# Kernel optimization log

Hardware: AMD Instinct MI355X
Metric: run time of the kernel (lower is better)

## Reference

```python
import jax, jax.numpy as jnp
import numpy as np
from jax import lax

NUM_HEADS = 8
KERNEL_SIZE = 7
PADDING_L = 3
EPS = 1e-12


def pow2_quantize(w):
    # LinearShift: weights constrained to sign * 2^round(log2|w|) (bit-shift arithmetic),
    # with straight-through estimator for gradients.
    wq = jnp.sign(w) * jnp.exp2(jnp.round(jnp.log2(jnp.abs(w) + EPS)))
    return w + lax.stop_gradient(wq - w)


def setup_inputs() -> dict:
    key = jax.random.key(0)
    k1, k2, k3 = jax.random.split(key, 3)
    T, B, C = 4096, 16, 512
    x = jax.random.normal(k1, (T, B, C), dtype=jnp.float32)
    shift_W = jax.random.normal(k2, (C, C), dtype=jnp.float32) * (1.0 / np.sqrt(C))
    shift_b = jnp.zeros((C,), dtype=jnp.float32)
    # xavier-uniform-ish init for the light-conv weight (H, K)
    lim = np.sqrt(6.0 / (NUM_HEADS + KERNEL_SIZE))
    weight = jax.random.uniform(k3, (NUM_HEADS, KERNEL_SIZE), minval=-lim, maxval=lim, dtype=jnp.float32)
    return {"x": x, "shift_W": shift_W, "shift_b": shift_b, "weight": weight}


def reference(x, shift_W, shift_b, weight):
    T, B, C = x.shape
    H, K = weight.shape
    R = C // H
    # 1) shift-linear: power-of-two quantized weights, y = x @ Wq^T + b  (T,B,C)
    Wq = pow2_quantize(shift_W)
    y = jnp.einsum("tbc,dc->tbd", x, Wq) + shift_b
    # 2) light (depthwise, head-shared) convolution along time
    xc = jnp.transpose(y, (1, 2, 0))  # (B, C, T)
    w = jax.nn.softmax(weight, axis=-1)  # weight_softmax=True
    # expand head kernels to per-channel depthwise kernels: (C, 1, K)
    w_full = jnp.repeat(w, R, axis=0)[:, None, :]
    out = lax.conv_general_dilated(
        xc, w_full,
        window_strides=(1,),
        padding=[(PADDING_L, K - 1 - PADDING_L)],
        dimension_numbers=("NCH", "OIH", "NCH"),
        feature_group_count=C,
    )  # (B, C, T)
    return jnp.transpose(out, (2, 0, 1))  # (T, B, C)
```

## Files before the change

kernel.cpp:

```cpp
#include <hip/hip_runtime.h>

constexpr int T_DIM = 4096;
constexpr int B_DIM = 16;
constexpr int C_DIM = 512;
constexpr int K_CONV = 7;
constexpr int M_DIM = T_DIM * B_DIM;
constexpr int BC = B_DIM * C_DIM;

typedef __attribute__((ext_vector_type(8))) short bf16x8;
typedef __attribute__((ext_vector_type(4))) float f32x4;
typedef __attribute__((ext_vector_type(8))) float f32x8;
typedef __attribute__((ext_vector_type(4))) unsigned int u32x4;

__device__ __forceinline__ unsigned short f2bf(float f) {
  unsigned u = __float_as_uint(f);
  u += 0x7fffu + ((u >> 16) & 1u);
  return (unsigned short)(u >> 16);
}
__device__ __forceinline__ unsigned pack2(float a, float b) {
  return (unsigned)f2bf(a) | (((unsigned)f2bf(b)) << 16);
}

__global__ __launch_bounds__(256) void quantize_w(
    const float* __restrict__ W, unsigned short* __restrict__ Wq) {
  int i = blockIdx.x * 256 + threadIdx.x;
  float w = W[i];
  float a = fabsf(w) + 1e-12f;
  float q = exp2f(rintf(log2f(a)));
  q = (w > 0.f) ? q : ((w < 0.f) ? -q : 0.f);
  Wq[i] = f2bf(q);
}

constexpr int BK = 32;
constexpr int NSTEP = C_DIM / BK;

__global__ __launch_bounds__(256, 4) void gemm_bt(
    const float* __restrict__ X, const short* __restrict__ Bt,
    const float* __restrict__ bias, unsigned short* __restrict__ Y) {
  constexpr int K = C_DIM, N = C_DIM;
  __shared__ __align__(16) short As[2][128 * BK];
  __shared__ __align__(16) short Bs[2][128 * BK];

  const int id   = blockIdx.x;
  const int xcd  = id & 7;
  const int slot = id >> 3;
  const int nb   = slot & 3;
  const int mb   = xcd * 64 + (slot >> 2);
  const int m0 = mb * 128;
  const int n0 = nb * 128;

  const int t    = threadIdx.x;
  const int lane = t & 63;
  const int wid  = t >> 6;

  const int ar = t >> 2;
  const int ac = (t & 3) * 8;
  const float* pA = X + (long)(m0 + ar) * K + ac;
  const int awoff = (((t & 3) ^ ((ar >> 1) & 3)) << 4);

  const int bc = ((t & 3) ^ ((t >> 3) & 3)) * 8;
  const short* pB = Bt + (long)(n0 + (t >> 2)) * K + bc;

  const int fr = lane & 15;
  const int fq = lane >> 4;
  const int wm = (wid >> 1) * 64;
  const int wn = (wid & 1) * 64;
  const int sw = ((fq ^ ((fr >> 1) & 3)) << 4);

  f32x4 ax[4];
  f32x4 acc[4][4] = {};

  auto loadA = [&](int k0) {
    ax[0] = *(const f32x4*)(pA + k0);
    ax[1] = *(const f32x4*)(pA + k0 + 4);
    ax[2] = *(const f32x4*)(pA + (long)64 * K + k0);
    ax[3] = *(const f32x4*)(pA + (long)64 * K + k0 + 4);
  };
  auto stageB = [&](int bsel, int k0) {
#pragma unroll
    for (int i = 0; i < 2; ++i)
      __builtin_amdgcn_global_load_lds(
          (const __attribute__((address_space(1))) void*)(pB + (long)i * 64 * K + k0),
          (__attribute__((address_space(3))) void*)&Bs[bsel][i * 2048 + wid * 512],
          16, 0, 0);
  };
  auto writeA = [&](int bsel) {
    char* base = (char*)&As[bsel][0];
    u32x4 p0, p1;
    p0[0] = pack2(ax[0][0], ax[0][1]);
    p0[1] = pack2(ax[0][2], ax[0][3]);
    p0[2] = pack2(ax[1][0], ax[1][1]);
    p0[3] = pack2(ax[1][2], ax[1][3]);
    p1[0] = pack2(ax[2][0], ax[2][1]);
    p1[1] = pack2(ax[2][2], ax[2][3]);
    p1[2] = pack2(ax[3][0], ax[3][1]);
    p1[3] = pack2(ax[3][2], ax[3][3]);
    *(u32x4*)(base + ar * 64 + awoff)        = p0;
    *(u32x4*)(base + (64 + ar) * 64 + awoff) = p1;
  };
  auto compute = [&](int bsel) {
    const char* ab = (const char*)&As[bsel][0];
    const char* bb = (const char*)&Bs[bsel][0];
    bf16x8 af[4], bfr[4];
#pragma unroll
    for (int i = 0; i < 4; ++i)
      af[i] = *(const bf16x8*)(ab + (wm + i * 16 + fr) * 64 + sw);
#pragma unroll
    for (int j = 0; j < 4; ++j)
      bfr[j] = *(const bf16x8*)(bb + (wn + j * 16 + fr) * 64 + sw);
#pragma unroll
    for (int i = 0; i < 4; ++i)
#pragma unroll
      for (int j = 0; j < 4; ++j)
        acc[i][j] = __builtin_amdgcn_mfma_f32_16x16x32_bf16(af[i], bfr[j], acc[i][j], 0, 0, 0);
  };

  loadA(0);
  stageB(0, 0);
  writeA(0);
  __syncthreads();

#pragma unroll
  for (int s = 0; s < NSTEP; ++s) {
    const int buf = s & 1;
    if (s + 1 < NSTEP) {
      loadA((s + 1) * BK);
      stageB(buf ^ 1, (s + 1) * BK);
    }
    compute(buf);
    if (s + 1 < NSTEP) {
      writeA(buf ^ 1);
      __syncthreads();
    }
  }

#pragma unroll
  for (int j = 0; j < 4; ++j) {
    const int gn = n0 + wn + j * 16 + fr;
    const float bv = bias[gn];
#pragma unroll
    for (int i = 0; i < 4; ++i) {
#pragma unroll
      for (int r = 0; r < 4; ++r) {
        const int gm = m0 + wm + i * 16 + fq * 4 + r;
        Y[(long)gm * N + gn] = f2bf(acc[i][j][r] + bv);
      }
    }
  }
}

__device__ __forceinline__ u32x4 loadY(const unsigned short* Y, int t, long off) {
  if ((unsigned)t < (unsigned)T_DIM)
    return *(const u32x4*)(Y + (long)t * BC + off);
  u32x4 z = {0u, 0u, 0u, 0u};
  return z;
}

__device__ __forceinline__ f32x8 unpack8(u32x4 u) {
  f32x8 r;
#pragma unroll
  for (int i = 0; i < 4; ++i) {
    unsigned w = u[i];
    r[2 * i]     = __uint_as_float(w << 16);
    r[2 * i + 1] = __uint_as_float(w & 0xffff0000u);
  }
  return r;
}

__global__ __launch_bounds__(256, 4) void lconv(
    const unsigned short* __restrict__ Y, const float* __restrict__ W,
    float* __restrict__ O) {
  __shared__ float sm_wf[8 * K_CONV];
  if (threadIdx.x < 8) {
    const int h = threadIdx.x;
    float v[K_CONV];
    float mx = -1e30f;
#pragma unroll
    for (int k = 0; k < K_CONV; ++k) { v[k] = W[h * K_CONV + k]; mx = fmaxf(mx, v[k]); }
    float s = 0.f;
#pragma unroll
    for (int k = 0; k < K_CONV; ++k) { v[k] = __expf(v[k] - mx); s += v[k]; }
    const float inv = 1.f / s;
#pragma unroll
    for (int k = 0; k < K_CONV; ++k) sm_wf[h * K_CONV + k] = v[k] * inv;
  }

  const int id   = blockIdx.x;
  const int xcd  = id & 7;
  const int slot = id >> 3;
  const int b    = slot >> 7;
  const int tl   = slot & 127;
  const int t    = xcd * 512 + tl * 4 + (threadIdx.x >> 6);
  const int cvec = threadIdx.x & 63;
  const long off = (long)b * C_DIM + cvec * 8;
  const int h    = cvec >> 3;

  u32x4 v[K_CONV];
#pragma unroll
  for (int k = 0; k < K_CONV; ++k) v[k] = loadY(Y, t + k - 3, off);

  __syncthreads();
  float wf[K_CONV];
#pragma unroll
  for (int k = 0; k < K_CONV; ++k) wf[k] = sm_wf[h * K_CONV + k];

  f32x8 acc = unpack8(v[0]) * wf[0];
#pragma unroll
  for (int k = 1; k < K_CONV; ++k) acc += unpack8(v[k]) * wf[k];

  float* op = O + (long)t * BC + off;
  *(f32x4*)op       = f32x4{acc[0], acc[1], acc[2], acc[3]};
  *(f32x4*)(op + 4) = f32x4{acc[4], acc[5], acc[6], acc[7]};
}

extern "C" void kernel_launch(void* const* d_in, const int* in_sizes, int n_in,
                              void* d_out, int out_size, void* d_ws, size_t ws_size,
                              hipStream_t stream) {
  const float* x       = (const float*)d_in[0];
  const float* shift_W = (const float*)d_in[1];
  const float* shift_b = (const float*)d_in[2];
  const float* weight  = (const float*)d_in[3];
  float* out = (float*)d_out;

  unsigned short* Wq = (unsigned short*)d_ws;
  unsigned short* Y  = Wq + C_DIM * C_DIM;

  quantize_w<<<(C_DIM * C_DIM) / 256, 256, 0, stream>>>(shift_W, Wq);
  gemm_bt<<<(M_DIM / 128) * (C_DIM / 128), 256, 0, stream>>>(
      x, (const short*)Wq, shift_b, Y);
  lconv<<<M_DIM * (C_DIM / 8) / 256, 256, 0, stream>>>(Y, weight, out);
}
```

Baseline: 296.6 us.

## Use 8-wave GEMM blocks and time-chunked light conv with register reuse

The GEMM block grows from 256 to 512 threads, so each of 8 waves computes a 64x32 sub-tile instead of 64x64 and each thread loads half as much A and B per step. This lowers register pressure and raises occupancy, but it also lowers the MFMA-to-LDS-read ratio per wave. The light conv kernel now has each thread compute 8 consecutive timesteps from 14 loaded rows instead of loading 7 rows per output. That removes most of the redundant overlapping Y reads, at the cost of more registers per thread and fewer blocks.

```diff
diff --git a/kernel.cpp b/kernel.cpp
--- a/kernel.cpp
+++ b/kernel.cpp
@@ -34,7 +34,7 @@
 constexpr int BK = 32;
 constexpr int NSTEP = C_DIM / BK;
 
-__global__ __launch_bounds__(256, 4) void gemm_bt(
+__global__ __launch_bounds__(512, 6) void gemm_bt(
     const float* __restrict__ X, const short* __restrict__ Bt,
     const float* __restrict__ bias, unsigned short* __restrict__ Y) {
   constexpr int K = C_DIM, N = C_DIM;
@@ -54,64 +54,54 @@
   const int wid  = t >> 6;
 
   const int ar = t >> 2;
-  const int ac = (t & 3) * 8;
-  const float* pA = X + (long)(m0 + ar) * K + ac;
+  const float* pA = X + (long)(m0 + ar) * K + (t & 3) * 8;
   const int awoff = (((t & 3) ^ ((ar >> 1) & 3)) << 4);
 
-  const int bc = ((t & 3) ^ ((t >> 3) & 3)) * 8;
-  const short* pB = Bt + (long)(n0 + (t >> 2)) * K + bc;
+  const int bc = ((lane & 3) ^ ((lane >> 3) & 3)) * 8;
+  const short* pB = Bt + (long)(n0 + wid * 16 + (lane >> 2)) * K + bc;
 
   const int fr = lane & 15;
   const int fq = lane >> 4;
-  const int wm = (wid >> 1) * 64;
-  const int wn = (wid & 1) * 64;
+  const int wm = (wid >> 2) * 64;
+  const int wn = (wid & 3) * 32;
   const int sw = ((fq ^ ((fr >> 1) & 3)) << 4);
 
-  f32x4 ax[4];
-  f32x4 acc[4][4] = {};
+  f32x4 ax[2];
+  f32x4 acc[4][2] = {};
 
   auto loadA = [&](int k0) {
     ax[0] = *(const f32x4*)(pA + k0);
     ax[1] = *(const f32x4*)(pA + k0 + 4);
-    ax[2] = *(const f32x4*)(pA + (long)64 * K + k0);
-    ax[3] = *(const f32x4*)(pA + (long)64 * K + k0 + 4);
   };
   auto stageB = [&](int bsel, int k0) {
-#pragma unroll
-    for (int i = 0; i < 2; ++i)
-      __builtin_amdgcn_global_load_lds(
-          (const __attribute__((address_space(1))) void*)(pB + (long)i * 64 * K + k0),
-          (__attribute__((address_space(3))) void*)&Bs[bsel][i * 2048 + wid * 512],
-          16, 0, 0);
+    __builtin_amdgcn_global_load_lds(
+        (const __attribute__((address_space(1))) void*)(pB + k0),
+        (__attribute__((address_space(3))) void*)&Bs[bsel][wid * 512],
+        16, 0, 0);
   };
   auto writeA = [&](int bsel) {
     char* base = (char*)&As[bsel][0];
-    u32x4 p0, p1;
-    p0[0] = pack2(ax[0][0], ax[0][1]);
-    p0[1] = pack2(ax[0][2], ax[0][3]);
-    p0[2] = pack2(ax[1][0], ax[1][1]);
-    p0[3] = pack2(ax[1][2], ax[1][3]);
-    p1[0] = pack2(ax[2][0], ax[2][1]);
-    p1[1] = pack2(ax[2][2], ax[2][3]);
-    p1[2] = pack2(ax[3][0], ax[3][1]);
-    p1[3] = pack2(ax[3][2], ax[3][3]);
-    *(u32x4*)(base + ar * 64 + awoff)        = p0;
-    *(u32x4*)(base + (64 + ar) * 64 + awoff) = p1;
+    u32x4 p;
+    p[0] = pack2(ax[0][0], ax[0][1]);
+    p[1] = pack2(ax[0][2], ax[0][3]);
+    p[2] = pack2(ax[1][0], ax[1][1]);
+    p[3] = pack2(ax[1][2], ax[1][3]);
+    *(u32x4*)(base + ar * 64 + awoff) = p;
   };
   auto compute = [&](int bsel) {
     const char* ab = (const char*)&As[bsel][0];
     const char* bb = (const char*)&Bs[bsel][0];
-    bf16x8 af[4], bfr[4];
+    bf16x8 af[4], bfr[2];
 #pragma unroll
     for (int i = 0; i < 4; ++i)
       af[i] = *(const bf16x8*)(ab + (wm + i * 16 + fr) * 64 + sw);
 #pragma unroll
-    for (int j = 0; j < 4; ++j)
+    for (int j = 0; j < 2; ++j)
       bfr[j] = *(const bf16x8*)(bb + (wn + j * 16 + fr) * 64 + sw);
 #pragma unroll
     for (int i = 0; i < 4; ++i)
 #pragma unroll
-      for (int j = 0; j < 4; ++j)
+      for (int j = 0; j < 2; ++j)
         acc[i][j] = __builtin_amdgcn_mfma_f32_16x16x32_bf16(af[i], bfr[j], acc[i][j], 0, 0, 0);
   };
 
@@ -135,7 +125,7 @@
   }
 
 #pragma unroll
-  for (int j = 0; j < 4; ++j) {
+  for (int j = 0; j < 2; ++j) {
     const int gn = n0 + wn + j * 16 + fr;
     const float bv = bias[gn];
 #pragma unroll
@@ -149,6 +139,8 @@
   }
 }
 
+constexpr int CHT = 8;
+
 __device__ __forceinline__ u32x4 loadY(const unsigned short* Y, int t, long off) {
   if ((unsigned)t < (unsigned)T_DIM)
     return *(const u32x4*)(Y + (long)t * BC + off);
@@ -167,7 +159,7 @@
   return r;
 }
 
-__global__ __launch_bounds__(256, 4) void lconv(
+__global__ __launch_bounds__(256, 6) void lconv(
     const unsigned short* __restrict__ Y, const float* __restrict__ W,
     float* __restrict__ O) {
   __shared__ float sm_wf[8 * K_CONV];
@@ -188,29 +180,31 @@
   const int id   = blockIdx.x;
   const int xcd  = id & 7;
   const int slot = id >> 3;
-  const int b    = slot >> 7;
-  const int tl   = slot & 127;
-  const int t    = xcd * 512 + tl * 4 + (threadIdx.x >> 6);
+  const int b    = slot >> 4;
+  const int tl   = slot & 15;
+  const int t0   = xcd * 512 + tl * 32 + (threadIdx.x >> 6) * CHT;
   const int cvec = threadIdx.x & 63;
   const long off = (long)b * C_DIM + cvec * 8;
   const int h    = cvec >> 3;
 
-  u32x4 v[K_CONV];
-#pragma unroll
-  for (int k = 0; k < K_CONV; ++k) v[k] = loadY(Y, t + k - 3, off);
+  u32x4 v[CHT + 6];
+#pragma unroll
+  for (int k = 0; k < CHT + 6; ++k) v[k] = loadY(Y, t0 - 3 + k, off);
 
   __syncthreads();
   float wf[K_CONV];
 #pragma unroll
   for (int k = 0; k < K_CONV; ++k) wf[k] = sm_wf[h * K_CONV + k];
 
-  f32x8 acc = unpack8(v[0]) * wf[0];
-#pragma unroll
-  for (int k = 1; k < K_CONV; ++k) acc += unpack8(v[k]) * wf[k];
-
-  float* op = O + (long)t * BC + off;
-  *(f32x4*)op       = f32x4{acc[0], acc[1], acc[2], acc[3]};
-  *(f32x4*)(op + 4) = f32x4{acc[4], acc[5], acc[6], acc[7]};
+#pragma unroll
+  for (int j = 0; j < CHT; ++j) {
+    f32x8 acc = unpack8(v[j]) * wf[0];
+#pragma unroll
+    for (int k = 1; k < K_CONV; ++k) acc += unpack8(v[j + k]) * wf[k];
+    float* op = O + (long)(t0 + j) * BC + off;
+    *(f32x4*)op       = f32x4{acc[0], acc[1], acc[2], acc[3]};
+    *(f32x4*)(op + 4) = f32x4{acc[4], acc[5], acc[6], acc[7]};
+  }
 }
 
 extern "C" void kernel_launch(void* const* d_in, const int* in_sizes, int n_in,
@@ -226,7 +220,7 @@
   unsigned short* Y  = Wq + C_DIM * C_DIM;
 
   quantize_w<<<(C_DIM * C_DIM) / 256, 256, 0, stream>>>(shift_W, Wq);
-  gemm_bt<<<(M_DIM / 128) * (C_DIM / 128), 256, 0, stream>>>(
+  gemm_bt<<<(M_DIM / 128) * (C_DIM / 128), 512, 0, stream>>>(
       x, (const short*)Wq, shift_b, Y);
-  lconv<<<M_DIM * (C_DIM / 8) / 256, 256, 0, stream>>>(Y, weight, out);
-}
+  lconv<<<M_DIM / CHT * (C_DIM / 8) / 256, 256, 0, stream>>>(Y, weight, out);
+}
```

After: 339.4 us. 1.14x slower.

## Triple-buffer GEMM shared-memory tiles with two-step-ahead prefetch and manual waitcnts

Applied to the files above, without the earlier changes.

The GEMM moves from double to triple buffering in LDS, issuing global loads for A and B two K-steps ahead. It uses explicit vmcnt/lgkmcnt waits and raw s_barrier instead of __syncthreads so more memory latency can overlap the MFMA work. Bias loads are hoisted to the kernel start. In exchange it needs more LDS and registers (occupancy hint drops from 4 to 3), and it depends on hand-counted vmcnt values being correct.

```diff
diff --git a/kernel.cpp b/kernel.cpp
--- a/kernel.cpp
+++ b/kernel.cpp
@@ -33,13 +33,14 @@
 
 constexpr int BK = 32;
 constexpr int NSTEP = C_DIM / BK;
-
-__global__ __launch_bounds__(256, 4) void gemm_bt(
+constexpr int NBUF = 3;
+
+__global__ __launch_bounds__(256, 3) void gemm_bt(
     const float* __restrict__ X, const short* __restrict__ Bt,
     const float* __restrict__ bias, unsigned short* __restrict__ Y) {
   constexpr int K = C_DIM, N = C_DIM;
-  __shared__ __align__(16) short As[2][128 * BK];
-  __shared__ __align__(16) short Bs[2][128 * BK];
+  __shared__ __align__(16) short As[NBUF][128 * BK];
+  __shared__ __align__(16) short Bs[NBUF][128 * BK];
 
   const int id   = blockIdx.x;
   const int xcd  = id & 7;
@@ -54,8 +55,7 @@
   const int wid  = t >> 6;
 
   const int ar = t >> 2;
-  const int ac = (t & 3) * 8;
-  const float* pA = X + (long)(m0 + ar) * K + ac;
+  const float* pA = X + (long)(m0 + ar) * K + (t & 3) * 8;
   const int awoff = (((t & 3) ^ ((ar >> 1) & 3)) << 4);
 
   const int bc = ((t & 3) ^ ((t >> 3) & 3)) * 8;
@@ -67,14 +67,19 @@
   const int wn = (wid & 1) * 64;
   const int sw = ((fq ^ ((fr >> 1) & 3)) << 4);
 
-  f32x4 ax[4];
+  float bv[4];
+#pragma unroll
+  for (int j = 0; j < 4; ++j) bv[j] = bias[n0 + wn + j * 16 + fr];
+  __builtin_amdgcn_sched_barrier(0);
+
+  f32x4 ax[2][4];
   f32x4 acc[4][4] = {};
 
-  auto loadA = [&](int k0) {
-    ax[0] = *(const f32x4*)(pA + k0);
-    ax[1] = *(const f32x4*)(pA + k0 + 4);
-    ax[2] = *(const f32x4*)(pA + (long)64 * K + k0);
-    ax[3] = *(const f32x4*)(pA + (long)64 * K + k0 + 4);
+  auto loadA = [&](int k0, int p) {
+    ax[p][0] = *(const f32x4*)(pA + k0);
+    ax[p][1] = *(const f32x4*)(pA + k0 + 4);
+    ax[p][2] = *(const f32x4*)(pA + (long)64 * K + k0);
+    ax[p][3] = *(const f32x4*)(pA + (long)64 * K + k0 + 4);
   };
   auto stageB = [&](int bsel, int k0) {
 #pragma unroll
@@ -84,19 +89,19 @@
           (__attribute__((address_space(3))) void*)&Bs[bsel][i * 2048 + wid * 512],
           16, 0, 0);
   };
-  auto writeA = [&](int bsel) {
+  auto writeA = [&](int bsel, int p) {
     char* base = (char*)&As[bsel][0];
-    u32x4 p0, p1;
-    p0[0] = pack2(ax[0][0], ax[0][1]);
-    p0[1] = pack2(ax[0][2], ax[0][3]);
-    p0[2] = pack2(ax[1][0], ax[1][1]);
-    p0[3] = pack2(ax[1][2], ax[1][3]);
-    p1[0] = pack2(ax[2][0], ax[2][1]);
-    p1[1] = pack2(ax[2][2], ax[2][3]);
-    p1[2] = pack2(ax[3][0], ax[3][1]);
-    p1[3] = pack2(ax[3][2], ax[3][3]);
-    *(u32x4*)(base + ar * 64 + awoff)        = p0;
-    *(u32x4*)(base + (64 + ar) * 64 + awoff) = p1;
+    u32x4 w0, w1;
+    w0[0] = pack2(ax[p][0][0], ax[p][0][1]);
+    w0[1] = pack2(ax[p][0][2], ax[p][0][3]);
+    w0[2] = pack2(ax[p][1][0], ax[p][1][1]);
+    w0[3] = pack2(ax[p][1][2], ax[p][1][3]);
+    w1[0] = pack2(ax[p][2][0], ax[p][2][1]);
+    w1[1] = pack2(ax[p][2][2], ax[p][2][3]);
+    w1[2] = pack2(ax[p][3][0], ax[p][3][1]);
+    w1[3] = pack2(ax[p][3][2], ax[p][3][3]);
+    *(u32x4*)(base + ar * 64 + awoff)        = w0;
+    *(u32x4*)(base + (64 + ar) * 64 + awoff) = w1;
   };
   auto compute = [&](int bsel) {
     const char* ab = (const char*)&As[bsel][0];
@@ -115,35 +120,47 @@
         acc[i][j] = __builtin_amdgcn_mfma_f32_16x16x32_bf16(af[i], bfr[j], acc[i][j], 0, 0, 0);
   };
 
-  loadA(0);
+  loadA(0, 0);
   stageB(0, 0);
-  writeA(0);
-  __syncthreads();
+  __builtin_amdgcn_sched_barrier(0);
+  loadA(BK, 1);
+  stageB(1, BK);
+  __builtin_amdgcn_sched_barrier(0);
+  asm volatile("s_waitcnt vmcnt(6)" ::: "memory");
+  writeA(0, 0);
+  asm volatile("s_waitcnt lgkmcnt(0)" ::: "memory");
+  __builtin_amdgcn_s_barrier();
+  __builtin_amdgcn_sched_barrier(0);
 
 #pragma unroll
   for (int s = 0; s < NSTEP; ++s) {
-    const int buf = s & 1;
+    if (s + 2 < NSTEP) {
+      loadA((s + 2) * BK, s & 1);
+      stageB((s + 2) % NBUF, (s + 2) * BK);
+      __builtin_amdgcn_sched_barrier(0);
+    }
+    compute(s % NBUF);
     if (s + 1 < NSTEP) {
-      loadA((s + 1) * BK);
-      stageB(buf ^ 1, (s + 1) * BK);
-    }
-    compute(buf);
-    if (s + 1 < NSTEP) {
-      writeA(buf ^ 1);
-      __syncthreads();
+      if (s + 2 < NSTEP)
+        asm volatile("s_waitcnt vmcnt(6)" ::: "memory");
+      else
+        asm volatile("s_waitcnt vmcnt(0)" ::: "memory");
+      writeA((s + 1) % NBUF, (s + 1) & 1);
+      asm volatile("s_waitcnt lgkmcnt(0)" ::: "memory");
+      __builtin_amdgcn_s_barrier();
+      __builtin_amdgcn_sched_barrier(0);
     }
   }
 
 #pragma unroll
   for (int j = 0; j < 4; ++j) {
     const int gn = n0 + wn + j * 16 + fr;
-    const float bv = bias[gn];
 #pragma unroll
     for (int i = 0; i < 4; ++i) {
 #pragma unroll
       for (int r = 0; r < 4; ++r) {
         const int gm = m0 + wm + i * 16 + fq * 4 + r;
-        Y[(long)gm * N + gn] = f2bf(acc[i][j][r] + bv);
+        Y[(long)gm * N + gn] = f2bf(acc[i][j][r] + bv[j]);
       }
     }
   }
```

New measurement: 301.8 us. About the same (+1.8%).

## Fuse light convolution into GEMM epilogue with time-chunked tiles and halo recompute

Applied to the files above, without the earlier changes.

Merges the GEMM and the depthwise time convolution into one kernel. Each block computes a 128-timestep tile for a single batch index, including a 3-step halo on each side, stages the bf16 result transposed in LDS, and applies the 7-tap softmax-weighted convolution before writing the final output. This removes the bf16 intermediate Y round trip through global memory and one kernel launch. In exchange, about 5% of the GEMM rows are recomputed for the halos, A-row loads are now strided by batch, and the output stores are scalar per channel.

```diff
diff --git a/kernel.cpp b/kernel.cpp
--- a/kernel.cpp
+++ b/kernel.cpp
@@ -4,13 +4,17 @@
 constexpr int B_DIM = 16;
 constexpr int C_DIM = 512;
 constexpr int K_CONV = 7;
-constexpr int M_DIM = T_DIM * B_DIM;
 constexpr int BC = B_DIM * C_DIM;
+constexpr int BK = 32;
+constexpr int NSTEP = C_DIM / BK;
+constexpr int TOUT = 122;
+constexpr int NCH = 34;
 
 typedef __attribute__((ext_vector_type(8))) short bf16x8;
 typedef __attribute__((ext_vector_type(4))) float f32x4;
 typedef __attribute__((ext_vector_type(8))) float f32x8;
 typedef __attribute__((ext_vector_type(4))) unsigned int u32x4;
+typedef __attribute__((ext_vector_type(2))) unsigned int u32x2;
 
 __device__ __forceinline__ unsigned short f2bf(float f) {
   unsigned u = __float_as_uint(f);
@@ -19,6 +23,16 @@
 }
 __device__ __forceinline__ unsigned pack2(float a, float b) {
   return (unsigned)f2bf(a) | (((unsigned)f2bf(b)) << 16);
+}
+__device__ __forceinline__ f32x8 unpack8(u32x4 u) {
+  f32x8 r;
+#pragma unroll
+  for (int i = 0; i < 4; ++i) {
+    unsigned w = u[i];
+    r[2 * i]     = __uint_as_float(w << 16);
+    r[2 * i + 1] = __uint_as_float(w & 0xffff0000u);
+  }
+  return r;
 }
 
 __global__ __launch_bounds__(256) void quantize_w(
@@ -31,35 +45,43 @@
   Wq[i] = f2bf(q);
 }
 
-constexpr int BK = 32;
-constexpr int NSTEP = C_DIM / BK;
-
-__global__ __launch_bounds__(256, 4) void gemm_bt(
+__global__ __launch_bounds__(256, 4) void gemm_conv(
     const float* __restrict__ X, const short* __restrict__ Bt,
-    const float* __restrict__ bias, unsigned short* __restrict__ Y) {
-  constexpr int K = C_DIM, N = C_DIM;
-  __shared__ __align__(16) short As[2][128 * BK];
-  __shared__ __align__(16) short Bs[2][128 * BK];
-
-  const int id   = blockIdx.x;
-  const int xcd  = id & 7;
-  const int slot = id >> 3;
-  const int nb   = slot & 3;
-  const int mb   = xcd * 64 + (slot >> 2);
-  const int m0 = mb * 128;
-  const int n0 = nb * 128;
+    const float* __restrict__ bias, const float* __restrict__ Wc,
+    float* __restrict__ Out) {
+  constexpr int K = C_DIM;
+  __shared__ __align__(16) short LdsU[16384];
+  short* const As0 = LdsU;
+  short* const As1 = LdsU + 4096;
+  short* const Bs0 = LdsU + 8192;
+  short* const Bs1 = LdsU + 12288;
+
+  const int id    = blockIdx.x;
+  const int xcd   = id & 7;
+  const int slot  = id >> 3;
+  const int np    = slot & 3;
+  const int cb    = xcd * 68 + (slot >> 2);
+  const int b     = cb & 15;
+  const int chunk = cb >> 4;
+  const int n0    = np * 128;
+  const int tstart = chunk * TOUT - 3;
 
   const int t    = threadIdx.x;
   const int lane = t & 63;
   const int wid  = t >> 6;
 
-  const int ar = t >> 2;
-  const int ac = (t & 3) * 8;
-  const float* pA = X + (long)(m0 + ar) * K + ac;
+  const int ar  = t >> 2;
+  const int acq = (t & 3) * 8;
+  const int tr0 = tstart + ar;
+  const int tr1 = tstart + 64 + ar;
+  const bool v0 = (unsigned)tr0 < (unsigned)T_DIM;
+  const bool v1 = (unsigned)tr1 < (unsigned)T_DIM;
+  const float* pA0 = X + (long)(v0 ? tr0 : 0) * BC + b * C_DIM + acq;
+  const float* pA1 = X + (long)(v1 ? tr1 : 0) * BC + b * C_DIM + acq;
   const int awoff = (((t & 3) ^ ((ar >> 1) & 3)) << 4);
 
-  const int bc = ((t & 3) ^ ((t >> 3) & 3)) * 8;
-  const short* pB = Bt + (long)(n0 + (t >> 2)) * K + bc;
+  const int bcs = ((t & 3) ^ ((t >> 3) & 3)) * 8;
+  const short* pB = Bt + (long)(n0 + (t >> 2)) * K + bcs;
 
   const int fr = lane & 15;
   const int fq = lane >> 4;
@@ -67,40 +89,45 @@
   const int wn = (wid & 1) * 64;
   const int sw = ((fq ^ ((fr >> 1) & 3)) << 4);
 
+  float bv[4];
+#pragma unroll
+  for (int j = 0; j < 4; ++j) bv[j] = bias[n0 + wn + j * 16 + fr];
+
   f32x4 ax[4];
   f32x4 acc[4][4] = {};
+  const f32x4 zf = {0.f, 0.f, 0.f, 0.f};
 
   auto loadA = [&](int k0) {
-    ax[0] = *(const f32x4*)(pA + k0);
-    ax[1] = *(const f32x4*)(pA + k0 + 4);
-    ax[2] = *(const f32x4*)(pA + (long)64 * K + k0);
-    ax[3] = *(const f32x4*)(pA + (long)64 * K + k0 + 4);
-  };
-  auto stageB = [&](int bsel, int k0) {
+    ax[0] = v0 ? *(const f32x4*)(pA0 + k0)     : zf;
+    ax[1] = v0 ? *(const f32x4*)(pA0 + k0 + 4) : zf;
+    ax[2] = v1 ? *(const f32x4*)(pA1 + k0)     : zf;
+    ax[3] = v1 ? *(const f32x4*)(pA1 + k0 + 4) : zf;
+  };
+  auto stageB = [&](short* bs, int k0) {
 #pragma unroll
     for (int i = 0; i < 2; ++i)
       __builtin_amdgcn_global_load_lds(
           (const __attribute__((address_space(1))) void*)(pB + (long)i * 64 * K + k0),
-          (__attribute__((address_space(3))) void*)&Bs[bsel][i * 2048 + wid * 512],
+          (__attribute__((address_space(3))) void*)&bs[i * 2048 + wid * 512],
           16, 0, 0);
   };
-  auto writeA = [&](int bsel) {
-    char* base = (char*)&As[bsel][0];
-    u32x4 p0, p1;
-    p0[0] = pack2(ax[0][0], ax[0][1]);
-    p0[1] = pack2(ax[0][2], ax[0][3]);
-    p0[2] = pack2(ax[1][0], ax[1][1]);
-    p0[3] = pack2(ax[1][2], ax[1][3]);
-    p1[0] = pack2(ax[2][0], ax[2][1]);
-    p1[1] = pack2(ax[2][2], ax[2][3]);
-    p1[2] = pack2(ax[3][0], ax[3][1]);
-    p1[3] = pack2(ax[3][2], ax[3][3]);
-    *(u32x4*)(base + ar * 64 + awoff)        = p0;
-    *(u32x4*)(base + (64 + ar) * 64 + awoff) = p1;
-  };
-  auto compute = [&](int bsel) {
-    const char* ab = (const char*)&As[bsel][0];
-    const char* bb = (const char*)&Bs[bsel][0];
+  auto writeA = [&](short* as) {
+    char* base = (char*)as;
+    u32x4 w0, w1;
+    w0[0] = pack2(ax[0][0], ax[0][1]);
+    w0[1] = pack2(ax[0][2], ax[0][3]);
+    w0[2] = pack2(ax[1][0], ax[1][1]);
+    w0[3] = pack2(ax[1][2], ax[1][3]);
+    w1[0] = pack2(ax[2][0], ax[2][1]);
+    w1[1] = pack2(ax[2][2], ax[2][3]);
+    w1[2] = pack2(ax[3][0], ax[3][1]);
+    w1[3] = pack2(ax[3][2], ax[3][3]);
+    *(u32x4*)(base + ar * 64 + awoff)        = w0;
+    *(u32x4*)(base + (64 + ar) * 64 + awoff) = w1;
+  };
+  auto compute = [&](const short* as, const short* bs) {
+    const char* ab = (const char*)as;
+    const char* bb = (const char*)bs;
     bf16x8 af[4], bfr[4];
 #pragma unroll
     for (int i = 0; i < 4; ++i)
@@ -116,101 +143,99 @@
   };
 
   loadA(0);
-  stageB(0, 0);
-  writeA(0);
+  stageB(Bs0, 0);
+  writeA(As0);
   __syncthreads();
 
 #pragma unroll
   for (int s = 0; s < NSTEP; ++s) {
-    const int buf = s & 1;
+    short* asC = (s & 1) ? As1 : As0;
+    short* bsC = (s & 1) ? Bs1 : Bs0;
+    short* asN = (s & 1) ? As0 : As1;
+    short* bsN = (s & 1) ? Bs0 : Bs1;
     if (s + 1 < NSTEP) {
       loadA((s + 1) * BK);
-      stageB(buf ^ 1, (s + 1) * BK);
-    }
-    compute(buf);
+      stageB(bsN, (s + 1) * BK);
+    }
+    compute(asC, bsC);
     if (s + 1 < NSTEP) {
-      writeA(buf ^ 1);
+      writeA(asN);
       __syncthreads();
     }
   }
 
+  __syncthreads();
+
+  const int cn  = t & 127;
+  const int dup = t >> 7;
+  const int hh  = (n0 + cn) >> 6;
+  float wf[K_CONV];
+  {
+    float mx = -1e30f;
+#pragma unroll
+    for (int k = 0; k < K_CONV; ++k) { wf[k] = Wc[hh * K_CONV + k]; mx = fmaxf(mx, wf[k]); }
+    float ssum = 0.f;
+#pragma unroll
+    for (int k = 0; k < K_CONV; ++k) { wf[k] = __expf(wf[k] - mx); ssum += wf[k]; }
+    const float inv = 1.f / ssum;
+#pragma unroll
+    for (int k = 0; k < K_CONV; ++k) wf[k] *= inv;
+  }
+
+  char* yt = (char*)LdsU;
+  const bool edge = (chunk == 0) | (chunk == NCH - 1);
 #pragma unroll
   for (int j = 0; j < 4; ++j) {
-    const int gn = n0 + wn + j * 16 + fr;
-    const float bv = bias[gn];
+    const int nrow = wn + j * 16 + fr;
 #pragma unroll
     for (int i = 0; i < 4; ++i) {
-#pragma unroll
-      for (int r = 0; r < 4; ++r) {
-        const int gm = m0 + wm + i * 16 + fq * 4 + r;
-        Y[(long)gm * N + gn] = f2bf(acc[i][j][r] + bv);
+      const int tcol = wm + i * 16 + fq * 4;
+      float e0 = acc[i][j][0] + bv[j];
+      float e1 = acc[i][j][1] + bv[j];
+      float e2 = acc[i][j][2] + bv[j];
+      float e3 = acc[i][j][3] + bv[j];
+      if (edge) {
+        const int tb = tstart + tcol;
+        e0 = ((unsigned)(tb + 0) < (unsigned)T_DIM) ? e0 : 0.f;
+        e1 = ((unsigned)(tb + 1) < (unsigned)T_DIM) ? e1 : 0.f;
+        e2 = ((unsigned)(tb + 2) < (unsigned)T_DIM) ? e2 : 0.f;
+        e3 = ((unsigned)(tb + 3) < (unsigned)T_DIM) ? e3 : 0.f;
       }
-    }
-  }
-}
-
-__device__ __forceinline__ u32x4 loadY(const unsigned short* Y, int t, long off) {
-  if ((unsigned)t < (unsigned)T_DIM)
-    return *(const u32x4*)(Y + (long)t * BC + off);
-  u32x4 z = {0u, 0u, 0u, 0u};
-  return z;
-}
-
-__device__ __forceinline__ f32x8 unpack8(u32x4 u) {
-  f32x8 r;
-#pragma unroll
-  for (int i = 0; i < 4; ++i) {
-    unsigned w = u[i];
-    r[2 * i]     = __uint_as_float(w << 16);
-    r[2 * i + 1] = __uint_as_float(w & 0xffff0000u);
-  }
-  return r;
-}
-
-__global__ __launch_bounds__(256, 4) void lconv(
-    const unsigned short* __restrict__ Y, const float* __restrict__ W,
-    float* __restrict__ O) {
-  __shared__ float sm_wf[8 * K_CONV];
-  if (threadIdx.x < 8) {
-    const int h = threadIdx.x;
-    float v[K_CONV];
-    float mx = -1e30f;
-#pragma unroll
-    for (int k = 0; k < K_CONV; ++k) { v[k] = W[h * K_CONV + k]; mx = fmaxf(mx, v[k]); }
-    float s = 0.f;
-#pragma unroll
-    for (int k = 0; k < K_CONV; ++k) { v[k] = __expf(v[k] - mx); s += v[k]; }
-    const float inv = 1.f / s;
-#pragma unroll
-    for (int k = 0; k < K_CONV; ++k) sm_wf[h * K_CONV + k] = v[k] * inv;
-  }
-
-  const int id   = blockIdx.x;
-  const int xcd  = id & 7;
-  const int slot = id >> 3;
-  const int b    = slot >> 7;
-  const int tl   = slot & 127;
-  const int t    = xcd * 512 + tl * 4 + (threadIdx.x >> 6);
-  const int cvec = threadIdx.x & 63;
-  const long off = (long)b * C_DIM + cvec * 8;
-  const int h    = cvec >> 3;
-
-  u32x4 v[K_CONV];
-#pragma unroll
-  for (int k = 0; k < K_CONV; ++k) v[k] = loadY(Y, t + k - 3, off);
-
+      u32x2 pw;
+      pw[0] = pack2(e0, e1);
+      pw[1] = pack2(e2, e3);
+      int byo = nrow * 256 + tcol * 2;
+      byo ^= (nrow & 7) << 4;
+      *(u32x2*)(yt + byo) = pw;
+    }
+  }
   __syncthreads();
-  float wf[K_CONV];
-#pragma unroll
-  for (int k = 0; k < K_CONV; ++k) wf[k] = sm_wf[h * K_CONV + k];
-
-  f32x8 acc = unpack8(v[0]) * wf[0];
-#pragma unroll
-  for (int k = 1; k < K_CONV; ++k) acc += unpack8(v[k]) * wf[k];
-
-  float* op = O + (long)t * BC + off;
-  *(f32x4*)op       = f32x4{acc[0], acc[1], acc[2], acc[3]};
-  *(f32x4*)(op + 4) = f32x4{acc[4], acc[5], acc[6], acc[7]};
+
+  const long obase = (long)b * C_DIM + n0 + cn;
+  const int swz = (cn & 7) << 4;
+#pragma unroll
+  for (int p = 0; p < 8; ++p) {
+    const int run = dup + 2 * p;
+    const int rb  = cn * 256 + run * 16;
+    u32x4 w0 = *(const u32x4*)(yt + (rb ^ swz));
+    u32x4 w1 = (run < 15) ? *(const u32x4*)(yt + ((rb + 16) ^ swz)) : w0;
+    f32x8 ya = unpack8(w0);
+    f32x8 yb = unpack8(w1);
+    float yw[16];
+#pragma unroll
+    for (int q = 0; q < 8; ++q) { yw[q] = ya[q]; yw[8 + q] = yb[q]; }
+#pragma unroll
+    for (int jj = 0; jj < 8; ++jj) {
+      const int lidx = run * 8 + jj;
+      const int tg   = chunk * TOUT + lidx;
+      if (lidx < TOUT && tg < T_DIM) {
+        float a = yw[jj] * wf[0];
+#pragma unroll
+        for (int k = 1; k < K_CONV; ++k) a += yw[jj + k] * wf[k];
+        Out[(long)tg * BC + obase] = a;
+      }
+    }
+  }
 }
 
 extern "C" void kernel_launch(void* const* d_in, const int* in_sizes, int n_in,
@@ -223,10 +248,8 @@
   float* out = (float*)d_out;
 
   unsigned short* Wq = (unsigned short*)d_ws;
-  unsigned short* Y  = Wq + C_DIM * C_DIM;
 
   quantize_w<<<(C_DIM * C_DIM) / 256, 256, 0, stream>>>(shift_W, Wq);
-  gemm_bt<<<(M_DIM / 128) * (C_DIM / 128), 256, 0, stream>>>(
-      x, (const short*)Wq, shift_b, Y);
-  lconv<<<M_DIM * (C_DIM / 8) / 256, 256, 0, stream>>>(Y, weight, out);
-}
+  gemm_conv<<<NCH * B_DIM * (C_DIM / 128), 256, 0, stream>>>(
+      x, (const short*)Wq, shift_b, weight, out);
+}
```

Result: slower. 346.9 us (+17.0%).
